# Performance work log

Measured on AMD Instinct MI355X. Metric: run time of the kernel, lower is better.

## Reference

```python
import jax, jax.numpy as jnp
import numpy as np

S = 128          # spatial grid size per axis
N = 100000       # active voxels
C_IN = 32
C_OUT = 32
FS = 3           # filter size per axis -> 27 offsets


def _build_rulebook():
    """Build submanifold-conv rulebook: for each active site and each of the
    27 filter offsets, the index of the active neighbor (or masked out)."""
    rng = np.random.default_rng(0)
    coords = rng.integers(0, S, size=(2 * N, 3))
    lin = coords[:, 0] * S * S + coords[:, 1] * S + coords[:, 2]
    lin = np.unique(lin)[:N]                      # sorted unique active sites
    xyz = np.stack([lin // (S * S), (lin // S) % S, lin % S], axis=1)  # [N,3]
    offs = np.stack(np.meshgrid(*([np.arange(FS) - FS // 2] * 3), indexing='ij'), -1).reshape(-1, 3)  # [27,3]
    nb = xyz[:, None, :] + offs[None, :, :]       # [N,27,3]
    inb = np.all((nb >= 0) & (nb < S), axis=-1)   # in-bounds
    nb_lin = nb[..., 0] * S * S + nb[..., 1] * S + nb[..., 2]
    pos = np.searchsorted(lin, nb_lin)
    pos_c = np.clip(pos, 0, N - 1)
    found = inb & (lin[pos_c] == nb_lin)
    nbr_idx = np.where(found, pos_c, 0).astype(np.int32)   # [N,27]
    return nbr_idx, found


def setup_inputs() -> dict:
    key = jax.random.key(0)
    k1, k2 = jax.random.split(key)
    nbr_idx, nbr_mask = _build_rulebook()
    K = FS ** 3
    std = (2.0 / C_IN / K) ** 0.5   # matches module init
    return {
        'features': jax.random.normal(k1, (N, C_IN), dtype=jnp.float32),
        'weight': std * jax.random.normal(k2, (K, C_IN, C_OUT), dtype=jnp.float32),
        'bias': jnp.zeros((C_OUT,), dtype=jnp.float32),
        'nbr_idx': jnp.asarray(nbr_idx),
        'nbr_mask': jnp.asarray(nbr_mask),
    }


def reference(features, weight, bias, nbr_idx, nbr_mask):
    # Submanifold sparse conv: gather active neighbors per filter offset,
    # multiply by per-offset [Cin,Cout] weight, accumulate at active sites.
    gathered = jnp.where(nbr_mask[:, :, None], features[nbr_idx], 0.0)  # [N,K,Cin]
    out = jnp.einsum('nki,kio->no', gathered, weight) + bias            # [N,Cout]
    return out
```

## Files before the change

### kernel.cpp

```cpp
#include <hip/hip_runtime.h>
#include <hip/hip_bf16.h>

#define NVOX 100000
#define CIN 32
#define COUT 32
#define KOFF 27
#define NTILE 6250

typedef __attribute__((ext_vector_type(8))) short short8;
typedef __attribute__((ext_vector_type(4))) float float4v;
typedef __attribute__((ext_vector_type(4))) int   int4v;

__global__ __launch_bounds__(512, 4) void subm_conv_kernel(
    const float* __restrict__ feat,
    const float* __restrict__ weight,
    const float* __restrict__ bias,
    const int* __restrict__ nbr_idx,
    const int* __restrict__ nbr_mask,
    float* __restrict__ out)
{
    __shared__ short8 wlds[KOFF * 2 * 64];
    __shared__ int    mstore[8 * 576];

    const int tid  = threadIdx.x;
    const int lane = tid & 63;
    const int wave = tid >> 6;
    const int m    = lane & 15;
    const int quad = lane >> 4;

    const int bid  = blockIdx.x;
    const int xcd  = bid & 7;
    const int bi   = bid >> 3;
    const int bswz = (xcd < 6) ? xcd * 98 + bi : 588 + (xcd - 6) * 97 + bi;

    const int tile0 = bswz * 8 + wave;
    const bool tv   = tile0 < NTILE;
    const int tile  = tv ? tile0 : (NTILE - 1);
    const int v0    = tile * 16;

    int* meta = mstore + wave * 576;
    {
        const int tb = v0 * KOFF;
        const int j0 = lane * 4;
        int4v ia = __builtin_nontemporal_load((const int4v*)(nbr_idx  + tb + j0));
        int4v ma = __builtin_nontemporal_load((const int4v*)(nbr_mask + tb + j0));
#pragma unroll
        for (int c = 0; c < 4; ++c) {
            int j = j0 + c;
            meta[(j / 27) * 28 + (j % 27)] = ma[c] ? (ia[c] << 7) : 1;
        }
        if (j0 < 176) {
            int4v ib = __builtin_nontemporal_load((const int4v*)(nbr_idx  + tb + 256 + j0));
            int4v mb = __builtin_nontemporal_load((const int4v*)(nbr_mask + tb + 256 + j0));
#pragma unroll
            for (int c = 0; c < 4; ++c) {
                int j = 256 + j0 + c;
                meta[(j / 27) * 28 + (j % 27)] = mb[c] ? (ib[c] << 7) : 1;
            }
        }
    }

    {
        const int co  = (tid & 15) + (((tid >> 6) & 1) << 4) * 0;
    }
#pragma unroll
    for (int u = 0; u < 7; ++u) {
        int g = tid + u * 512;
        if (g < KOFF * 2 * 64) {
            int k   = g >> 7;
            int rem = g & 127;
            int t   = rem >> 6;
            int ln  = rem & 63;
            int co  = t * 16 + (ln & 15);
            int cib = (ln >> 4) * 8;
            const float* wp = weight + (k * CIN + cib) * COUT + co;
            union { short8 s8; __bf16 b[8]; } cw;
#pragma unroll
            for (int j = 0; j < 8; ++j) cw.b[j] = (__bf16)wp[j * COUT];
            wlds[g] = cw.s8;
        }
    }

    int enc[28];
    {
        const int4v* mp = (const int4v*)(meta + m * 28);
#pragma unroll
        for (int i = 0; i < 7; ++i) {
            int4v t = mp[i];
            enc[i * 4 + 0] = t.x; enc[i * 4 + 1] = t.y;
            enc[i * 4 + 2] = t.z; enc[i * 4 + 3] = t.w;
        }
    }

    unsigned bmv = 0;
#pragma unroll
    for (int k = 0; k < KOFF; ++k)
        bmv |= (__any(!(enc[k] & 1)) ? 1u : 0u) << k;
    const unsigned bm = (unsigned)__builtin_amdgcn_readfirstlane((int)bmv);

    const char* fb   = (const char*)feat;
    const int   boff = quad * 32;

    float4v a0[6], a1[6];
#pragma unroll
    for (int k = 0; k < 6; ++k) {
        unsigned e = (unsigned)enc[k];
        const char* p = fb + (e & ~127u) + boff;
        a0[k] = *(const float4v*)p;
        a1[k] = *(const float4v*)(p + 16);
    }

    __syncthreads();

    float4v acc0 = {0.f, 0.f, 0.f, 0.f};
    float4v acc1 = {0.f, 0.f, 0.f, 0.f};

#pragma unroll
    for (int k = 0; k < KOFF; ++k) {
        const int slot = k % 6;
        float4v f0 = a0[slot];
        float4v f1 = a1[slot];
        const unsigned ecur = (unsigned)enc[k];
        if (k + 6 < KOFF) {
            unsigned en = (unsigned)enc[k + 6];
            const char* pn = fb + (en & ~127u) + boff;
            a0[slot] = *(const float4v*)pn;
            a1[slot] = *(const float4v*)(pn + 16);
        }

        if (bm & (1u << k)) {
            union { short8 s8; unsigned u4[4]; __bf16 b[8]; } cu;
            cu.b[0] = (__bf16)f0.x; cu.b[1] = (__bf16)f0.y;
            cu.b[2] = (__bf16)f0.z; cu.b[3] = (__bf16)f0.w;
            cu.b[4] = (__bf16)f1.x; cu.b[5] = (__bf16)f1.y;
            cu.b[6] = (__bf16)f1.z; cu.b[7] = (__bf16)f1.w;
            if (ecur & 1u) {
                cu.u4[0] = 0; cu.u4[1] = 0; cu.u4[2] = 0; cu.u4[3] = 0;
            }
            short8 a = cu.s8;
            short8 wb0 = wlds[k * 128 + lane];
            short8 wb1 = wlds[k * 128 + 64 + lane];
            acc0 = __builtin_amdgcn_mfma_f32_16x16x32_bf16(a, wb0, acc0, 0, 0, 0);
            acc1 = __builtin_amdgcn_mfma_f32_16x16x32_bf16(a, wb1, acc1, 0, 0, 0);
        }
    }

    float* tb = (float*)(mstore + wave * 576);

    const float bs0 = bias[m];
    const float bs1 = bias[16 + m];
    if (tv) {
#pragma unroll
        for (int r = 0; r < 4; ++r) {
            tb[(quad * 4 + r) * 36 + m]      = acc0[r] + bs0;
            tb[(quad * 4 + r) * 36 + 16 + m] = acc1[r] + bs1;
        }
#pragma unroll
        for (int p = 0; p < 2; ++p) {
            int flat = p * 64 + lane;
            int row  = flat >> 3;
            int ch   = flat & 7;
            float4v val = *(const float4v*)(tb + row * 36 + ch * 4);
            __builtin_nontemporal_store(val, (float4v*)(out + (size_t)(v0 + row) * COUT + ch * 4));
        }
    }
}

extern "C" void kernel_launch(void* const* d_in, const int* in_sizes, int n_in,
                              void* d_out, int out_size, void* d_ws, size_t ws_size,
                              hipStream_t stream) {
    const float* feat = (const float*)d_in[0];
    const float* wgt  = (const float*)d_in[1];
    const float* bias = (const float*)d_in[2];
    const int*   nidx = (const int*)d_in[3];
    const int*   nmsk = (const int*)d_in[4];
    float*       out  = (float*)d_out;

    const int block = 512;
    const int grid  = (NTILE + 7) / 8;
    subm_conv_kernel<<<grid, block, 0, stream>>>(feat, wgt, bias, nidx, nmsk, out);
}
```

Measured before the change: 108.6 us.

## Precompute bf16 weight fragments in a prep kernel and prefetch them early

Adds a small kernel that converts the fp32 weights into bf16 MFMA fragment layout once per call and writes them into the workspace. The main kernel now loads the prepared short8 fragments into registers early and stores them to LDS after the rulebook decode, instead of having every block do strided fp32 loads and conversions. Masked neighbours now point at the tile's own voxel rather than row 0, which spreads out dummy loads, and the bias load is hoisted ahead of the barrier. The cost is an extra kernel launch and more register pressure from holding the prefetched fragments.

Result: no change. 107.8 us (-0.7%).

```diff
diff --git a/kernel.cpp b/kernel.cpp
--- a/kernel.cpp
+++ b/kernel.cpp
@@ -11,9 +11,27 @@
 typedef __attribute__((ext_vector_type(4))) float float4v;
 typedef __attribute__((ext_vector_type(4))) int   int4v;
 
+__global__ __launch_bounds__(256) void wfrag_kernel(
+    const float* __restrict__ weight, short8* __restrict__ wfrag)
+{
+    int g = blockIdx.x * 256 + threadIdx.x;
+    if (g >= KOFF * 2 * 64) return;
+    int k   = g >> 7;
+    int rem = g & 127;
+    int t   = rem >> 6;
+    int ln  = rem & 63;
+    int co  = t * 16 + (ln & 15);
+    int cib = (ln >> 4) * 8;
+    const float* wp = weight + (k * CIN + cib) * COUT + co;
+    union { short8 s8; __bf16 b[8]; } cw;
+#pragma unroll
+    for (int j = 0; j < 8; ++j) cw.b[j] = (__bf16)wp[j * COUT];
+    wfrag[g] = cw.s8;
+}
+
 __global__ __launch_bounds__(512, 4) void subm_conv_kernel(
     const float* __restrict__ feat,
-    const float* __restrict__ weight,
+    const short8* __restrict__ wfrag,
     const float* __restrict__ bias,
     const int* __restrict__ nbr_idx,
     const int* __restrict__ nbr_mask,
@@ -38,16 +56,24 @@
     const int tile  = tv ? tile0 : (NTILE - 1);
     const int v0    = tile * 16;
 
+    short8 wreg[7];
+#pragma unroll
+    for (int u = 0; u < 7; ++u) {
+        int g = tid + u * 512;
+        if (g < KOFF * 2 * 64) wreg[u] = wfrag[g];
+    }
+
     int* meta = mstore + wave * 576;
     {
         const int tb = v0 * KOFF;
         const int j0 = lane * 4;
+        const int deadv = (v0 << 7) | 1;
         int4v ia = __builtin_nontemporal_load((const int4v*)(nbr_idx  + tb + j0));
         int4v ma = __builtin_nontemporal_load((const int4v*)(nbr_mask + tb + j0));
 #pragma unroll
         for (int c = 0; c < 4; ++c) {
             int j = j0 + c;
-            meta[(j / 27) * 28 + (j % 27)] = ma[c] ? (ia[c] << 7) : 1;
+            meta[(j / 27) * 28 + (j % 27)] = ma[c] ? (ia[c] << 7) : deadv;
         }
         if (j0 < 176) {
             int4v ib = __builtin_nontemporal_load((const int4v*)(nbr_idx  + tb + 256 + j0));
@@ -55,29 +81,8 @@
 #pragma unroll
             for (int c = 0; c < 4; ++c) {
                 int j = 256 + j0 + c;
-                meta[(j / 27) * 28 + (j % 27)] = mb[c] ? (ib[c] << 7) : 1;
+                meta[(j / 27) * 28 + (j % 27)] = mb[c] ? (ib[c] << 7) : deadv;
             }
-        }
-    }
-
-    {
-        const int co  = (tid & 15) + (((tid >> 6) & 1) << 4) * 0;
-    }
-#pragma unroll
-    for (int u = 0; u < 7; ++u) {
-        int g = tid + u * 512;
-        if (g < KOFF * 2 * 64) {
-            int k   = g >> 7;
-            int rem = g & 127;
-            int t   = rem >> 6;
-            int ln  = rem & 63;
-            int co  = t * 16 + (ln & 15);
-            int cib = (ln >> 4) * 8;
-            const float* wp = weight + (k * CIN + cib) * COUT + co;
-            union { short8 s8; __bf16 b[8]; } cw;
-#pragma unroll
-            for (int j = 0; j < 8; ++j) cw.b[j] = (__bf16)wp[j * COUT];
-            wlds[g] = cw.s8;
         }
     }
 
@@ -98,17 +103,25 @@
         bmv |= (__any(!(enc[k] & 1)) ? 1u : 0u) << k;
     const unsigned bm = (unsigned)__builtin_amdgcn_readfirstlane((int)bmv);
 
+#pragma unroll
+    for (int u = 0; u < 7; ++u) {
+        int g = tid + u * 512;
+        if (g < KOFF * 2 * 64) wlds[g] = wreg[u];
+    }
+
     const char* fb   = (const char*)feat;
     const int   boff = quad * 32;
 
     float4v a0[6], a1[6];
 #pragma unroll
     for (int k = 0; k < 6; ++k) {
-        unsigned e = (unsigned)enc[k];
-        const char* p = fb + (e & ~127u) + boff;
+        const char* p = fb + (size_t)((unsigned)enc[k] & ~127u) + boff;
         a0[k] = *(const float4v*)p;
         a1[k] = *(const float4v*)(p + 16);
     }
+
+    const float bs0 = bias[m];
+    const float bs1 = bias[16 + m];
 
     __syncthreads();
 
@@ -122,8 +135,7 @@
         float4v f1 = a1[slot];
         const unsigned ecur = (unsigned)enc[k];
         if (k + 6 < KOFF) {
-            unsigned en = (unsigned)enc[k + 6];
-            const char* pn = fb + (en & ~127u) + boff;
+            const char* pn = fb + (size_t)((unsigned)enc[k + 6] & ~127u) + boff;
             a0[slot] = *(const float4v*)pn;
             a1[slot] = *(const float4v*)(pn + 16);
         }
@@ -147,8 +159,6 @@
 
     float* tb = (float*)(mstore + wave * 576);
 
-    const float bs0 = bias[m];
-    const float bs1 = bias[16 + m];
     if (tv) {
 #pragma unroll
         for (int r = 0; r < 4; ++r) {
@@ -176,7 +186,11 @@
     const int*   nmsk = (const int*)d_in[4];
     float*       out  = (float*)d_out;
 
+    short8* wfrag = (short8*)d_ws;
+
+    wfrag_kernel<<<14, 256, 0, stream>>>(wgt, wfrag);
+
     const int block = 512;
     const int grid  = (NTILE + 7) / 8;
-    subm_conv_kernel<<<grid, block, 0, stream>>>(feat, wgt, bias, nidx, nmsk, out);
+    subm_conv_kernel<<<grid, block, 0, stream>>>(feat, wfrag, bias, nidx, nmsk, out);
 }
```
